# Performance work log

Measured on AMD Instinct MI355X. Metric: run time of the kernel, lower is better.

The kernel has to match this reference:

```python
import jax, jax.numpy as jnp
import numpy as np
from jax import lax

TAU_MIN = 0.01
TAU_MAX = 10.0
SLOW_TAU = 5.0


def setup_inputs() -> dict:
    key = jax.random.key(0)
    ks = iter(jax.random.split(key, 40))
    def p(shape, scale=0.05):
        return (jax.random.normal(next(ks), shape, jnp.float32) * scale)
    B, T, D = 1024, 512, 31
    FU, SU, H = 32, 32, 64
    inp = {
        "x": jax.random.normal(next(ks), (B, T, D), jnp.float32),
        # FlashFloodGate: Linear(62->32), Linear(32->1)
        "fg_w1": p((32, 2 * D)), "fg_b1": p((32,)),
        "fg_w2": p((1, 32)), "fg_b2": p((1,)),
        # fast LTC cell
        "fwin": p((FU, D)), "fbin": p((FU,)), "fwrec": p((FU, FU)),
        # slow LTC cell
        "swin": p((SU, D)), "sbin": p((SU,)), "swrec": p((SU, SU)),
        # fusion Linear(64->64)
        "fu_w": p((H, FU + SU)), "fu_b": p((H,)),
        # attention Linear(64->32), Linear(32->1)
        "at_w1": p((32, H)), "at_b1": p((32,)),
        "at_w2": p((1, 32)), "at_b2": p((1,)),
        # depth head Linear(64->64), Linear(64->5)
        "d_w1": p((64, H)), "d_b1": p((64,)),
        "d_w2": p((5, 64)), "d_b2": p((5,)),
        # overflow head Linear(64->64), Linear(64->32), Linear(32->1)
        "o_w1": p((64, H)), "o_b1": p((64,)),
        "o_w2": p((32, 64)), "o_b2": p((32,)),
        "o_w3": p((1, 32)), "o_b3": p((1,)),
        # intensity head Linear(64->32), Linear(32->1)
        "i_w1": p((32, H)), "i_b1": p((32,)),
        "i_w2": p((1, 32)), "i_b2": p((1,)),
    }
    return inp


def _ltc_scan(pre_tbh, w_rec, tau_tb1, h0):
    # pre_tbh: [T,B,H] precomputed W_in x + b; tau_tb1 broadcastable to [T,B,1]
    def step(h, inp):
        pre_t, tau_t = inp
        upd = jnp.tanh(pre_t + h @ w_rec.T)
        h = h + (upd - h) / tau_t
        return h, h
    _, hs = lax.scan(step, h0, (pre_tbh, tau_tb1))
    return jnp.transpose(hs, (1, 0, 2))  # [B,T,H]


def _forward(x, fg_w1, fg_b1, fg_w2, fg_b2, fwin, fbin, fwrec, swin, sbin, swrec,
             fu_w, fu_b, at_w1, at_b1, at_w2, at_b2, d_w1, d_b1, d_w2, d_b2,
             o_w1, o_b1, o_w2, o_b2, o_w3, o_b3, i_w1, i_b1, i_w2, i_b2):
    B, T, D = x.shape
    # FlashFloodGate over all timesteps (x_prev of t=0 is x_0 -> dx=0)
    dx = jnp.concatenate([jnp.zeros_like(x[:, :1]), x[:, 1:] - x[:, :-1]], axis=1)
    ci = jnp.concatenate([x, dx], axis=-1)                       # [B,T,2D]
    cs = jax.nn.sigmoid(jnp.tanh(ci @ fg_w1.T + fg_b1) @ fg_w2.T + fg_b2)  # [B,T,1]
    tau_fast = TAU_MAX - cs * (TAU_MAX - TAU_MIN)                # [B,T,1]
    # fast LTC (stepwise tau)
    pre_f = jnp.transpose(x @ fwin.T + fbin, (1, 0, 2))          # [T,B,FU]
    fast = _ltc_scan(pre_f, fwrec, jnp.transpose(tau_fast, (1, 0, 2)),
                     jnp.zeros((B, fwrec.shape[0]), x.dtype))
    # slow LTC (constant tau = 5.0, shape [B,1])
    pre_s = jnp.transpose(x @ swin.T + sbin, (1, 0, 2))          # [T,B,SU]
    slow = _ltc_scan(pre_s, swrec, jnp.full((T, 1, 1), SLOW_TAU, x.dtype),
                     jnp.zeros((B, swrec.shape[0]), x.dtype))
    # fusion
    ltc = jnp.tanh(jnp.concatenate([fast, slow], axis=-1) @ fu_w.T + fu_b)  # [B,T,H]
    # attention over time
    logits = jnp.tanh(ltc @ at_w1.T + at_b1) @ at_w2.T + at_b2   # [B,T,1]
    attn = jax.nn.softmax(logits, axis=1)
    context = jnp.sum(ltc * attn, axis=1)                        # [B,H]
    # heads (dropout is identity in eval)
    depths = jax.nn.relu(context @ d_w1.T + d_b1) @ d_w2.T + d_b2
    overflow = jax.nn.sigmoid(
        jax.nn.relu(jax.nn.relu(context @ o_w1.T + o_b1) @ o_w2.T + o_b2) @ o_w3.T + o_b3)
    intensity = jax.nn.sigmoid(jax.nn.relu(context @ i_w1.T + i_b1) @ i_w2.T + i_b2)
    return (depths, overflow, intensity)


def reference(x, fg_w1, fg_b1, fg_w2, fg_b2, fwin, fbin, fwrec, swin, sbin, swrec,
              fu_w, fu_b, at_w1, at_b1, at_w2, at_b2, d_w1, d_b1, d_w2, d_b2,
              o_w1, o_b1, o_w2, o_b2, o_w3, o_b3, i_w1, i_b1, i_w2, i_b2):
    return _forward(x, fg_w1, fg_b1, fg_w2, fg_b2, fwin, fbin, fwrec, swin, sbin,
                    swrec, fu_w, fu_b, at_w1, at_b1, at_w2, at_b2, d_w1, d_b1,
                    d_w2, d_b2, o_w1, o_b1, o_w2, o_b2, o_w3, o_b3,
                    i_w1, i_b1, i_w2, i_b2)
```

## Files before the change

kernel.cpp:

```cpp
#include <hip/hip_runtime.h>


#define T_  512
#define D_  31
#define GR_ 8
#define NG_ 64
#define NIT 70
#define L2E 1.4426950408889634f

typedef decltype(__builtin_amdgcn_cvt_pkrtz(0.0f, 0.0f)) h2;
typedef _Float16 h8v __attribute__((ext_vector_type(8)));
typedef float    f4v __attribute__((ext_vector_type(4)));

__device__ __forceinline__ float fexp2(float x){ return __builtin_amdgcn_exp2f(x); }
__device__ __forceinline__ float frcp (float x){ return __builtin_amdgcn_rcpf(x); }
__device__ __forceinline__ float fast_tanh(float x){
    float e = fexp2(x * 2.8853900817779268f);
    return 1.0f - 2.0f * frcp(1.0f + e);
}
__device__ __forceinline__ h2 cvt2(float a, float b){ return __builtin_amdgcn_cvt_pkrtz(a, b); }
__device__ __forceinline__ h2 bch2(unsigned v){ return __builtin_bit_cast(h2, v); }
__device__ __forceinline__ unsigned bcu(h2 v){ return __builtin_bit_cast(unsigned, v); }

template <int CTRL>
__device__ __forceinline__ float dppf(float v){
    int r = __builtin_amdgcn_update_dpp(0, __builtin_bit_cast(int, v),
                                        CTRL, 0xf, 0xf, true);
    return __builtin_bit_cast(float, r);
}
template <int CTRL>
__device__ __forceinline__ unsigned dppu(unsigned v){
    return (unsigned)__builtin_amdgcn_update_dpp(0, (int)v, CTRL, 0xf, 0xf, true);
}
__device__ __forceinline__ unsigned swz16(unsigned v){
    return (unsigned)__builtin_amdgcn_ds_swizzle((int)v, 0x401F);
}
__device__ __forceinline__ float rsum16(float v){
    v += dppf<0xB1>(v); v += dppf<0x4E>(v); v += dppf<0x141>(v); v += dppf<0x140>(v);
    return v;
}

#if __has_builtin(__builtin_amdgcn_fdot2)
#define FDOT2(acc, a, b) (acc) = __builtin_amdgcn_fdot2((a), (b), (acc), false)
#else
#define FDOT2(acc, a, b) (acc) += (float)(a)[0]*(float)(b)[0] + (float)(a)[1]*(float)(b)[1]
#endif

#define MFMA16(A, Bf, Cf) __builtin_amdgcn_mfma_f32_16x16x32_f16((A), (Bf), (Cf), 0, 0, 0)

#define BAR() do { asm volatile("s_waitcnt lgkmcnt(0)" ::: "memory"); \
                   __builtin_amdgcn_s_barrier();                      \
                   asm volatile("" ::: "memory"); } while (0)

__launch_bounds__(256, 4)
__global__ void lnn_mf(
    const float* __restrict__ X,
    const float* __restrict__ fg_w1, const float* __restrict__ fg_b1,
    const float* __restrict__ fg_w2, const float* __restrict__ fg_b2,
    const float* __restrict__ fwin,  const float* __restrict__ fbin,
    const float* __restrict__ fwrec,
    const float* __restrict__ swin,  const float* __restrict__ sbin,
    const float* __restrict__ swrec,
    const float* __restrict__ fu_w,  const float* __restrict__ fu_b,
    const float* __restrict__ at_w1, const float* __restrict__ at_b1,
    const float* __restrict__ at_w2, const float* __restrict__ at_b2,
    const float* __restrict__ d_w1,  const float* __restrict__ d_b1,
    const float* __restrict__ d_w2,  const float* __restrict__ d_b2,
    const float* __restrict__ o_w1,  const float* __restrict__ o_b1,
    const float* __restrict__ o_w2,  const float* __restrict__ o_b2,
    const float* __restrict__ o_w3,  const float* __restrict__ o_b3,
    const float* __restrict__ i_w1,  const float* __restrict__ i_b1,
    const float* __restrict__ i_w2,  const float* __restrict__ i_b2,
    float* __restrict__ out, int B)
{
    const int b    = blockIdx.x;
    const int tx   = threadIdx.x;
    const int wid  = tx >> 6;
    const int lane = tx & 63;
    const int u    = lane & 31;
    const int hb32 = lane & 32;
    const int role = (wid + b) & 3;

    __shared__ __align__(16) float    xr_sh [4][GR_][36];
    __shared__ float    xdm   [36];
    __shared__ float    pre_sh[4][GR_][65];
    __shared__ float    rt_sh [4][GR_];
    __shared__ __align__(16) unsigned hpk_sh[4][GR_][36];
    __shared__ __align__(16) unsigned ltcpk [4][GR_][36];
    __shared__ float    pw_sh [16];
    __shared__ float    ctx_sh[64];

    if (tx < 32) xr_sh[tx >> 3][tx & 7][31] = 0.0f;

    if (role == 0) {
        const int col = lane & 15, kb = lane >> 4;
        h8v wB[8];
        #pragma unroll
        for (int c = 0; c < 8; ++c) {
            float wv[8];
            #pragma unroll
            for (int j = 0; j < 8; ++j) {
                const int k = kb*8 + j;
                float v = 0.0f;
                if (k < 31) {
                    const int uu = 16*(c & 1) + col;
                    if (c < 2)      v = fg_w1[uu*62 + k] + fg_w1[uu*62 + 31 + k];
                    else if (c < 4) v = fg_w1[uu*62 + 31 + k];
                    else if (c < 6) v = fwin[uu*31 + k];
                    else            v = swin[uu*31 + k];
                }
                wv[j] = v;
            }
            uint4 qq = { bcu(cvt2(wv[0],wv[1])), bcu(cvt2(wv[2],wv[3])),
                         bcu(cvt2(wv[4],wv[5])), bcu(cvt2(wv[6],wv[7])) };
            wB[c] = __builtin_bit_cast(h8v, qq);
        }
        const float b1c[2] = { fg_b1[col], fg_b1[16 + col] };
        const float pb[4]  = { fbin[col], fbin[16+col], sbin[col], sbin[16+col] };
        const float w2n[2] = { fg_w2[col] * (-L2E), fg_w2[16+col] * (-L2E) };
        const float b2n    = fg_b2[0] * (-L2E);
        const unsigned* Xu = (const unsigned*)(X + (size_t)b * T_ * D_ + lane);
        float ypv[2] = {0.0f, 0.0f};
        asm volatile("s_waitcnt vmcnt(0)" ::: "memory");

        #pragma unroll
        for (int gg = 0; gg < 2; ++gg)
            #pragma unroll
            for (int k = 0; k < GR_; ++k)
                if (lane < 31)
                    __builtin_amdgcn_global_load_lds(
                        (const __attribute__((address_space(1))) unsigned*)(Xu + (size_t)(GR_*gg + k) * 31),
                        (__attribute__((address_space(3))) unsigned*)(&xr_sh[gg][k][0]),
                        4, 0, 0);

        for (int i = 0; i < NIT; ++i) {
            asm volatile("s_waitcnt vmcnt(8)" ::: "memory");
            BAR();
            {
                const int gq = i + 2;
                #pragma unroll
                for (int k = 0; k < GR_; ++k) {
                    int tl = GR_*gq + k; if (tl > 511) tl = 511;
                    float* dst = (gq <= NG_-1) ? &xr_sh[gq & 3][k][0] : &xdm[0];
                    if (lane < 31)
                        __builtin_amdgcn_global_load_lds(
                            (const __attribute__((address_space(1))) unsigned*)(Xu + (size_t)tl * 31),
                            (__attribute__((address_space(3))) unsigned*)dst,
                            4, 0, 0);
                }
            }
            if ((i & 1) && i <= NG_-1) {
                const int sA_ = (i-1) & 3, sB_ = i & 3;
                const float* xrow = (col < 8) ? &xr_sh[sA_][col][kb*8]
                                              : &xr_sh[sB_][col-8][kb*8];
                float4 xa = *(const float4*)xrow;
                float4 xb = *(const float4*)(xrow + 4);
                uint4 aq = { bcu(cvt2(xa.x,xa.y)), bcu(cvt2(xa.z,xa.w)),
                             bcu(cvt2(xb.x,xb.y)), bcu(cvt2(xb.z,xb.w)) };
                h8v Af = __builtin_bit_cast(h8v, aq);
                f4v C[8];
                #pragma unroll
                for (int c = 0; c < 8; ++c) {
                    f4v z = {0.f, 0.f, 0.f, 0.f};
                    C[c] = MFMA16(Af, wB[c], z);
                }
                const int tslot = (kb < 2) ? sA_ : sB_;
                const int tb    = (kb & 1) * 4;
                float tp[4] = {0.f, 0.f, 0.f, 0.f};
                #pragma unroll
                for (int p = 0; p < 2; ++p) {
                    f4v G = C[p], Y = C[2+p];
                    if (i == 1) ypv[p] = __shfl(Y[0], col);
                    float ylast = __shfl(Y[3], 48 + col);
                    float yup   = __shfl(Y[3], (lane - 16) & 63);
                    float ysh0  = (kb == 0) ? ypv[p] : yup;
                    float h1v[4];
                    h1v[0] = fast_tanh(G[0] - ysh0 + b1c[p]);
                    h1v[1] = fast_tanh(G[1] - Y[0] + b1c[p]);
                    h1v[2] = fast_tanh(G[2] - Y[1] + b1c[p]);
                    h1v[3] = fast_tanh(G[3] - Y[2] + b1c[p]);
                    ypv[p] = ylast;
                    #pragma unroll
                    for (int r = 0; r < 4; ++r) tp[r] += h1v[r] * w2n[p];
                }
                #pragma unroll
                for (int r = 0; r < 4; ++r) {
                    float s  = rsum16(tp[r]) + b2n;
                    float cs = frcp(1.0f + fexp2(s));
                    float rt = frcp(10.0f - 9.99f * cs);
                    if (col == 0) rt_sh[tslot][tb + r] = rt;
                }
                #pragma unroll
                for (int c = 4; c < 8; ++c) {
                    const int uo = (c < 6 ? 0 : 32) + 16*(c & 1) + col;
                    #pragma unroll
                    for (int r = 0; r < 4; ++r)
                        pre_sh[tslot][tb + r][uo] = C[c][r] + pb[c-4];
                }
            }
        }
        asm volatile("s_waitcnt vmcnt(0)" ::: "memory");
    } else if (role == 1) {
        const bool slow = (lane >= 32);
        const float* W  = (slow ? swrec : fwrec) + u * 32;
        const int M0[8] = {0,2,7,5,15,13,8,10};
        const int M1[8] = {1,3,6,4,14,12,9,11};
        h2 wr[16];
        #pragma unroll
        for (int j = 0; j < 16; ++j) {
            const int x = (j & 8) ? 16 : 0;
            wr[j] = cvt2(W[u ^ M0[j & 7] ^ x], W[u ^ M1[j & 7] ^ x]);
        }
        float h_st = 0.0f;

        for (int i = 0; i < NIT; ++i) {
            BAR();
            if (i >= 2 && i <= NG_ + 1) {
                const int sR = (i - 2) & 3;
                float preA[8], rtA[8];
                #pragma unroll
                for (int k = 0; k < GR_; ++k) {
                    preA[k] = pre_sh[sR][k][lane];
                    rtA[k]  = slow ? 0.2f : rt_sh[sR][k];
                }
                __builtin_amdgcn_s_setprio(1);
                #pragma unroll
                for (int k = 0; k < GR_; ++k) {
                    float hn = dppf<0xB1>(h_st);
                    unsigned u0 = bcu(cvt2(h_st, hn));
                    unsigned u1 = dppu<0x4E>(u0);
                    unsigned u2 = dppu<0x141>(u0);
                    unsigned u3 = dppu<0x141>(u1);
                    unsigned u4 = dppu<0x140>(u0);
                    unsigned u5 = dppu<0x140>(u1);
                    unsigned u6 = dppu<0x140>(u2);
                    unsigned u7 = dppu<0x140>(u3);
                    unsigned u8  = swz16(u0), u9  = swz16(u1);
                    unsigned u10 = swz16(u2), u11 = swz16(u3);
                    unsigned u12 = swz16(u4), u13 = swz16(u5);
                    unsigned u14 = swz16(u6), u15 = swz16(u7);
                    float a0 = 0.f, a1 = 0.f, a2 = 0.f, a3 = 0.f;
                    FDOT2(a0, bch2(u0),  wr[0]);  FDOT2(a1, bch2(u1),  wr[1]);
                    FDOT2(a2, bch2(u2),  wr[2]);  FDOT2(a3, bch2(u3),  wr[3]);
                    FDOT2(a0, bch2(u4),  wr[4]);  FDOT2(a1, bch2(u5),  wr[5]);
                    FDOT2(a2, bch2(u6),  wr[6]);  FDOT2(a3, bch2(u7),  wr[7]);
                    FDOT2(a0, bch2(u8),  wr[8]);  FDOT2(a1, bch2(u9),  wr[9]);
                    FDOT2(a2, bch2(u10), wr[10]); FDOT2(a3, bch2(u11), wr[11]);
                    FDOT2(a0, bch2(u12), wr[12]); FDOT2(a1, bch2(u13), wr[13]);
                    FDOT2(a2, bch2(u14), wr[14]); FDOT2(a3, bch2(u15), wr[15]);
                    float v   = (a0 + a1) + (a2 + a3);
                    float upd = fast_tanh(v + preA[k]);
                    h_st += (upd - h_st) * rtA[k];
                    float hw = dppf<0xB1>(h_st);
                    if (!(lane & 1))
                        hpk_sh[sR][k][lane >> 1] = bcu(cvt2(h_st, hw));
                }
                __builtin_amdgcn_s_setprio(0);
            }
        }
    } else if (role == 2) {
        const int col = lane & 15, kb = lane >> 4;
        h8v wF[8];
        #pragma unroll
        for (int kc = 0; kc < 2; ++kc)
            #pragma unroll
            for (int nc = 0; nc < 4; ++nc) {
                float wv[8];
                #pragma unroll
                for (int j = 0; j < 8; ++j)
                    wv[j] = fu_w[(16*nc + col)*64 + 32*kc + 8*kb + j];
                uint4 qq = { bcu(cvt2(wv[0],wv[1])), bcu(cvt2(wv[2],wv[3])),
                             bcu(cvt2(wv[4],wv[5])), bcu(cvt2(wv[6],wv[7])) };
                wF[kc*4 + nc] = __builtin_bit_cast(h8v, qq);
            }
        const float fb4[4] = { fu_b[col], fu_b[16+col], fu_b[32+col], fu_b[48+col] };

        for (int i = 0; i < NIT; ++i) {
            BAR();
            if ((i & 1) && i >= 5 && i <= 67) {
                const int s0 = (i-5) & 3, s1 = (i-4) & 3;
                const unsigned* hrow = (col < 8) ? &hpk_sh[s0][col][0]
                                                 : &hpk_sh[s1][col-8][0];
                uint4 a0q = *(const uint4*)(hrow + kb*4);
                uint4 a1q = *(const uint4*)(hrow + kb*4 + 16);
                h8v A0 = __builtin_bit_cast(h8v, a0q);
                h8v A1 = __builtin_bit_cast(h8v, a1q);
                const int tslot = (kb < 2) ? s0 : s1;
                const int tb    = (kb & 1) * 4;
                #pragma unroll
                for (int nc = 0; nc < 4; ++nc) {
                    f4v c4 = {0.f, 0.f, 0.f, 0.f};
                    c4 = MFMA16(A0, wF[nc],     c4);
                    c4 = MFMA16(A1, wF[4 + nc], c4);
                    #pragma unroll
                    for (int r = 0; r < 4; ++r) {
                        float v  = fast_tanh(c4[r] + fb4[nc]);
                        float vn = dppf<0xB1>(v);
                        h2 pk = (col & 1) ? cvt2(vn, v) : cvt2(v, vn);
                        if (!(col & 1))
                            ltcpk[tslot][tb + r][(16*nc + col) >> 1] = bcu(pk);
                    }
                }
            }
        }
    } else {
        const int col = lane & 15, kb = lane >> 4;
        h8v wA[4];
        #pragma unroll
        for (int kt = 0; kt < 2; ++kt)
            #pragma unroll
            for (int nt = 0; nt < 2; ++nt) {
                float wv[8];
                #pragma unroll
                for (int j = 0; j < 8; ++j)
                    wv[j] = at_w1[(nt*16 + col)*64 + kt*32 + 8*kb + j];
                uint4 qq = { bcu(cvt2(wv[0],wv[1])), bcu(cvt2(wv[2],wv[3])),
                             bcu(cvt2(wv[4],wv[5])), bcu(cvt2(wv[6],wv[7])) };
                wA[kt*2 + nt] = __builtin_bit_cast(h8v, qq);
            }
        const float ab1v[2] = { at_b1[col], at_b1[16 + col] };
        const float w2L[2]  = { at_w2[col] * L2E, at_w2[16 + col] * L2E };
        const float ab2L    = at_b2[0] * L2E;
        float s_run = 0.0f, c_run = 0.0f;

        for (int i = 0; i < NIT; ++i) {
            BAR();
            if ((i & 1) && i >= 7) {
                const int s0 = (i-7) & 3, s1 = (i-6) & 3;
                const unsigned* lrow = (col < 8) ? &ltcpk[s0][col][0]
                                                 : &ltcpk[s1][col-8][0];
                uint4 l0q = *(const uint4*)(lrow + kb*4);
                uint4 l1q = *(const uint4*)(lrow + kb*4 + 16);
                h8v L0 = __builtin_bit_cast(h8v, l0q);
                h8v L1 = __builtin_bit_cast(h8v, l1q);
                f4v CA[2];
                #pragma unroll
                for (int nt = 0; nt < 2; ++nt) {
                    f4v c4 = {0.f, 0.f, 0.f, 0.f};
                    c4 = MFMA16(L0, wA[nt],     c4);
                    c4 = MFMA16(L1, wA[2 + nt], c4);
                    CA[nt] = c4;
                }
                #pragma unroll
                for (int r = 0; r < 4; ++r) {
                    float s = fast_tanh(CA[0][r] + ab1v[0]) * w2L[0]
                            + fast_tanh(CA[1][r] + ab1v[1]) * w2L[1];
                    s = rsum16(s);
                    float pw = fexp2(s + ab2L);
                    if (col == 0) pw_sh[kb*4 + r] = pw;
                }
                #pragma unroll
                for (int t = 0; t < 16; ++t) {
                    const int sl = (t < 8) ? s0 : s1;
                    const int tr = t & 7;
                    float ltc = (float)((const _Float16*)(&ltcpk[sl][tr][0]))[lane];
                    float pwv = pw_sh[t];
                    s_run += pwv;
                    c_run += pwv * ltc;
                }
            }
        }
        ctx_sh[lane] = c_run * frcp(s_run);
    }

    __syncthreads();

    if (wid == 0) {
        float r1 = d_b1[lane];
        #pragma unroll
        for (int c = 0; c < 16; ++c) {
            float4 cq = ((const float4*)ctx_sh)[c];
            float4 wq = ((const float4*)(d_w1 + lane*64))[c];
            r1 += wq.x*cq.x + wq.y*cq.y + wq.z*cq.z + wq.w*cq.w;
        }
        r1 = fmaxf(r1, 0.0f);
        #pragma unroll
        for (int kk = 0; kk < 5; ++kk) {
            float v = d_w2[kk*64 + lane] * r1;
            v += __shfl_xor(v, 1);  v += __shfl_xor(v, 2);
            v += __shfl_xor(v, 4);  v += __shfl_xor(v, 8);
            v += __shfl_xor(v, 16); v += __shfl_xor(v, 32);
            if (lane == 0) out[b*5 + kk] = v + d_b2[kk];
        }
    } else if (wid == 1) {
        float r1 = o_b1[lane];
        #pragma unroll
        for (int c = 0; c < 16; ++c) {
            float4 cq = ((const float4*)ctx_sh)[c];
            float4 wq = ((const float4*)(o_w1 + lane*64))[c];
            r1 += wq.x*cq.x + wq.y*cq.y + wq.z*cq.z + wq.w*cq.w;
        }
        r1 = fmaxf(r1, 0.0f);
        float acc = 0.0f;
        #pragma unroll
        for (int j = 0; j < 32; ++j) {
            float rj = __shfl(r1, hb32 + j);
            acc += o_w2[u*64 + hb32 + j] * rj;
        }
        acc += __shfl_xor(acc, 32);
        float r2 = fmaxf(acc + o_b2[u], 0.0f);
        float v  = o_w3[u] * r2;
        v += __shfl_xor(v, 1);  v += __shfl_xor(v, 2);
        v += __shfl_xor(v, 4);  v += __shfl_xor(v, 8);
        v += __shfl_xor(v, 16);
        if (lane == 0) {
            float e = fexp2((v + o_b3[0]) * -L2E);
            out[5*B + b] = frcp(1.0f + e);
        }
    } else if (wid == 2) {
        float acc = 0.0f;
        #pragma unroll
        for (int c = 0; c < 8; ++c) {
            float4 cq = ((const float4*)(ctx_sh + hb32))[c];
            float4 wq = ((const float4*)(i_w1 + u*64 + hb32))[c];
            acc += wq.x*cq.x + wq.y*cq.y + wq.z*cq.z + wq.w*cq.w;
        }
        acc += __shfl_xor(acc, 32);
        float r1 = fmaxf(acc + i_b1[u], 0.0f);
        float v  = i_w2[u] * r1;
        v += __shfl_xor(v, 1);  v += __shfl_xor(v, 2);
        v += __shfl_xor(v, 4);  v += __shfl_xor(v, 8);
        v += __shfl_xor(v, 16);
        if (lane == 0) {
            float e = fexp2((v + i_b2[0]) * -L2E);
            out[6*B + b] = frcp(1.0f + e);
        }
    }
}

extern "C" void kernel_launch(void* const* d_in, const int* in_sizes, int n_in,
                              void* d_out, int out_size, void* d_ws, size_t ws_size,
                              hipStream_t stream) {
    (void)n_in; (void)out_size; (void)d_ws; (void)ws_size;
    const float* X     = (const float*)d_in[0];
    const float* fg_w1 = (const float*)d_in[1];
    const float* fg_b1 = (const float*)d_in[2];
    const float* fg_w2 = (const float*)d_in[3];
    const float* fg_b2 = (const float*)d_in[4];
    const float* fwin  = (const float*)d_in[5];
    const float* fbin  = (const float*)d_in[6];
    const float* fwrec = (const float*)d_in[7];
    const float* swin  = (const float*)d_in[8];
    const float* sbin  = (const float*)d_in[9];
    const float* swrec = (const float*)d_in[10];
    const float* fu_w  = (const float*)d_in[11];
    const float* fu_b  = (const float*)d_in[12];
    const float* at_w1 = (const float*)d_in[13];
    const float* at_b1 = (const float*)d_in[14];
    const float* at_w2 = (const float*)d_in[15];
    const float* at_b2 = (const float*)d_in[16];
    const float* d_w1  = (const float*)d_in[17];
    const float* d_b1  = (const float*)d_in[18];
    const float* d_w2  = (const float*)d_in[19];
    const float* d_b2  = (const float*)d_in[20];
    const float* o_w1  = (const float*)d_in[21];
    const float* o_b1  = (const float*)d_in[22];
    const float* o_w2  = (const float*)d_in[23];
    const float* o_b2  = (const float*)d_in[24];
    const float* o_w3  = (const float*)d_in[25];
    const float* o_b3  = (const float*)d_in[26];
    const float* i_w1  = (const float*)d_in[27];
    const float* i_b1  = (const float*)d_in[28];
    const float* i_w2  = (const float*)d_in[29];
    const float* i_b2  = (const float*)d_in[30];
    float* out = (float*)d_out;

    const int B = in_sizes[0] / (T_ * D_);
    dim3 grid(B), block(256);
    hipLaunchKernelGGL(lnn_mf, grid, block, 0, stream,
        X, fg_w1, fg_b1, fg_w2, fg_b2, fwin, fbin, fwrec, swin, sbin, swrec,
        fu_w, fu_b, at_w1, at_b1, at_w2, at_b2, d_w1, d_b1, d_w2, d_b2,
        o_w1, o_b1, o_w2, o_b2, o_w3, o_b3, i_w1, i_b1, i_w2, i_b2, out, B);
}
```

Measured before the change: 111.0 us.

## Double timestep group size to halve pipeline barriers and simplify stage scheduling

Raises each pipeline stage's group from 8 to 16 timesteps, so the warp-specialized pipeline runs 36 barrier iterations instead of 70. Stages now work every iteration on one full 16-row group instead of pairing two 8-row groups on alternate iterations, and the h and ltc staging buffers shrink to double buffers. The recurrence also builds its upper-half operands with DPP ops from a single swizzled value instead of eight swizzles. In exchange, the recurrence does more serial steps per iteration while the other stages wait, and register pressure rises from the larger preA/rtA arrays.

```diff
diff --git a/kernel.cpp b/kernel.cpp
--- a/kernel.cpp
+++ b/kernel.cpp
@@ -3,9 +3,9 @@
 
 #define T_  512
 #define D_  31
-#define GR_ 8
-#define NG_ 64
-#define NIT 70
+#define GR_ 16
+#define NG_ 32
+#define NIT 36
 #define L2E 1.4426950408889634f
 
 typedef decltype(__builtin_amdgcn_cvt_pkrtz(0.0f, 0.0f)) h2;
@@ -85,12 +85,12 @@
     __shared__ float    xdm   [36];
     __shared__ float    pre_sh[4][GR_][65];
     __shared__ float    rt_sh [4][GR_];
-    __shared__ __align__(16) unsigned hpk_sh[4][GR_][36];
-    __shared__ __align__(16) unsigned ltcpk [4][GR_][36];
-    __shared__ float    pw_sh [16];
+    __shared__ __align__(16) unsigned hpk_sh[2][GR_][36];
+    __shared__ __align__(16) unsigned ltcpk [2][GR_][36];
+    __shared__ float    pw_sh [GR_];
     __shared__ float    ctx_sh[64];
 
-    if (tx < 32) xr_sh[tx >> 3][tx & 7][31] = 0.0f;
+    if (tx < 64) xr_sh[tx >> 4][tx & 15][31] = 0.0f;
 
     if (role == 0) {
         const int col = lane & 15, kb = lane >> 4;
@@ -134,7 +134,7 @@
                         4, 0, 0);
 
         for (int i = 0; i < NIT; ++i) {
-            asm volatile("s_waitcnt vmcnt(8)" ::: "memory");
+            asm volatile("s_waitcnt vmcnt(16)" ::: "memory");
             BAR();
             {
                 const int gq = i + 2;
@@ -149,10 +149,9 @@
                             4, 0, 0);
                 }
             }
-            if ((i & 1) && i <= NG_-1) {
-                const int sA_ = (i-1) & 3, sB_ = i & 3;
-                const float* xrow = (col < 8) ? &xr_sh[sA_][col][kb*8]
-                                              : &xr_sh[sB_][col-8][kb*8];
+            if (i <= NG_-1) {
+                const int sG = i & 3;
+                const float* xrow = &xr_sh[sG][col][kb*8];
                 float4 xa = *(const float4*)xrow;
                 float4 xb = *(const float4*)(xrow + 4);
                 uint4 aq = { bcu(cvt2(xa.x,xa.y)), bcu(cvt2(xa.z,xa.w)),
@@ -164,13 +163,12 @@
                     f4v z = {0.f, 0.f, 0.f, 0.f};
                     C[c] = MFMA16(Af, wB[c], z);
                 }
-                const int tslot = (kb < 2) ? sA_ : sB_;
-                const int tb    = (kb & 1) * 4;
+                const int tb = kb * 4;
                 float tp[4] = {0.f, 0.f, 0.f, 0.f};
                 #pragma unroll
                 for (int p = 0; p < 2; ++p) {
                     f4v G = C[p], Y = C[2+p];
-                    if (i == 1) ypv[p] = __shfl(Y[0], col);
+                    if (i == 0) ypv[p] = __shfl(Y[0], col);
                     float ylast = __shfl(Y[3], 48 + col);
                     float yup   = __shfl(Y[3], (lane - 16) & 63);
                     float ysh0  = (kb == 0) ? ypv[p] : yup;
@@ -188,14 +186,14 @@
                     float s  = rsum16(tp[r]) + b2n;
                     float cs = frcp(1.0f + fexp2(s));
                     float rt = frcp(10.0f - 9.99f * cs);
-                    if (col == 0) rt_sh[tslot][tb + r] = rt;
+                    if (col == 0) rt_sh[sG][tb + r] = rt;
                 }
                 #pragma unroll
                 for (int c = 4; c < 8; ++c) {
                     const int uo = (c < 6 ? 0 : 32) + 16*(c & 1) + col;
                     #pragma unroll
                     for (int r = 0; r < 4; ++r)
-                        pre_sh[tslot][tb + r][uo] = C[c][r] + pb[c-4];
+                        pre_sh[sG][tb + r][uo] = C[c][r] + pb[c-4];
                 }
             }
         }
@@ -216,8 +214,10 @@
         for (int i = 0; i < NIT; ++i) {
             BAR();
             if (i >= 2 && i <= NG_ + 1) {
-                const int sR = (i - 2) & 3;
-                float preA[8], rtA[8];
+                const int gR = i - 2;
+                const int sR = gR & 3;
+                const int sH = gR & 1;
+                float preA[GR_], rtA[GR_];
                 #pragma unroll
                 for (int k = 0; k < GR_; ++k) {
                     preA[k] = pre_sh[sR][k][lane];
@@ -228,6 +228,7 @@
                 for (int k = 0; k < GR_; ++k) {
                     float hn = dppf<0xB1>(h_st);
                     unsigned u0 = bcu(cvt2(h_st, hn));
+                    unsigned w0 = swz16(u0);
                     unsigned u1 = dppu<0x4E>(u0);
                     unsigned u2 = dppu<0x141>(u0);
                     unsigned u3 = dppu<0x141>(u1);
@@ -235,25 +236,28 @@
                     unsigned u5 = dppu<0x140>(u1);
                     unsigned u6 = dppu<0x140>(u2);
                     unsigned u7 = dppu<0x140>(u3);
-                    unsigned u8  = swz16(u0), u9  = swz16(u1);
-                    unsigned u10 = swz16(u2), u11 = swz16(u3);
-                    unsigned u12 = swz16(u4), u13 = swz16(u5);
-                    unsigned u14 = swz16(u6), u15 = swz16(u7);
+                    unsigned w1 = dppu<0x4E>(w0);
+                    unsigned w2 = dppu<0x141>(w0);
+                    unsigned w3 = dppu<0x141>(w1);
+                    unsigned w4 = dppu<0x140>(w0);
+                    unsigned w5 = dppu<0x140>(w1);
+                    unsigned w6 = dppu<0x140>(w2);
+                    unsigned w7 = dppu<0x140>(w3);
                     float a0 = 0.f, a1 = 0.f, a2 = 0.f, a3 = 0.f;
-                    FDOT2(a0, bch2(u0),  wr[0]);  FDOT2(a1, bch2(u1),  wr[1]);
-                    FDOT2(a2, bch2(u2),  wr[2]);  FDOT2(a3, bch2(u3),  wr[3]);
-                    FDOT2(a0, bch2(u4),  wr[4]);  FDOT2(a1, bch2(u5),  wr[5]);
-                    FDOT2(a2, bch2(u6),  wr[6]);  FDOT2(a3, bch2(u7),  wr[7]);
-                    FDOT2(a0, bch2(u8),  wr[8]);  FDOT2(a1, bch2(u9),  wr[9]);
-                    FDOT2(a2, bch2(u10), wr[10]); FDOT2(a3, bch2(u11), wr[11]);
-                    FDOT2(a0, bch2(u12), wr[12]); FDOT2(a1, bch2(u13), wr[13]);
-                    FDOT2(a2, bch2(u14), wr[14]); FDOT2(a3, bch2(u15), wr[15]);
+                    FDOT2(a0, bch2(u0), wr[0]);  FDOT2(a1, bch2(u1), wr[1]);
+                    FDOT2(a2, bch2(u2), wr[2]);  FDOT2(a3, bch2(u3), wr[3]);
+                    FDOT2(a0, bch2(u4), wr[4]);  FDOT2(a1, bch2(u5), wr[5]);
+                    FDOT2(a2, bch2(u6), wr[6]);  FDOT2(a3, bch2(u7), wr[7]);
+                    FDOT2(a0, bch2(w0), wr[8]);  FDOT2(a1, bch2(w1), wr[9]);
+                    FDOT2(a2, bch2(w2), wr[10]); FDOT2(a3, bch2(w3), wr[11]);
+                    FDOT2(a0, bch2(w4), wr[12]); FDOT2(a1, bch2(w5), wr[13]);
+                    FDOT2(a2, bch2(w6), wr[14]); FDOT2(a3, bch2(w7), wr[15]);
                     float v   = (a0 + a1) + (a2 + a3);
                     float upd = fast_tanh(v + preA[k]);
                     h_st += (upd - h_st) * rtA[k];
                     float hw = dppf<0xB1>(h_st);
                     if (!(lane & 1))
-                        hpk_sh[sR][k][lane >> 1] = bcu(cvt2(h_st, hw));
+                        hpk_sh[sH][k][lane >> 1] = bcu(cvt2(h_st, hw));
                 }
                 __builtin_amdgcn_s_setprio(0);
             }
@@ -277,16 +281,15 @@
 
         for (int i = 0; i < NIT; ++i) {
             BAR();
-            if ((i & 1) && i >= 5 && i <= 67) {
-                const int s0 = (i-5) & 3, s1 = (i-4) & 3;
-                const unsigned* hrow = (col < 8) ? &hpk_sh[s0][col][0]
-                                                 : &hpk_sh[s1][col-8][0];
+            if (i >= 3 && i <= NG_ + 2) {
+                const int gF = i - 3;
+                const int sH = gF & 1;
+                const unsigned* hrow = &hpk_sh[sH][col][0];
                 uint4 a0q = *(const uint4*)(hrow + kb*4);
                 uint4 a1q = *(const uint4*)(hrow + kb*4 + 16);
                 h8v A0 = __builtin_bit_cast(h8v, a0q);
                 h8v A1 = __builtin_bit_cast(h8v, a1q);
-                const int tslot = (kb < 2) ? s0 : s1;
-                const int tb    = (kb & 1) * 4;
+                const int tb = kb * 4;
                 #pragma unroll
                 for (int nc = 0; nc < 4; ++nc) {
                     f4v c4 = {0.f, 0.f, 0.f, 0.f};
@@ -298,7 +301,7 @@
                         float vn = dppf<0xB1>(v);
                         h2 pk = (col & 1) ? cvt2(vn, v) : cvt2(v, vn);
                         if (!(col & 1))
-                            ltcpk[tslot][tb + r][(16*nc + col) >> 1] = bcu(pk);
+                            ltcpk[gF & 1][tb + r][(16*nc + col) >> 1] = bcu(pk);
                     }
                 }
             }
@@ -325,10 +328,10 @@
 
         for (int i = 0; i < NIT; ++i) {
             BAR();
-            if ((i & 1) && i >= 7) {
-                const int s0 = (i-7) & 3, s1 = (i-6) & 3;
-                const unsigned* lrow = (col < 8) ? &ltcpk[s0][col][0]
-                                                 : &ltcpk[s1][col-8][0];
+            if (i >= 4) {
+                const int gA = i - 4;
+                const int sl = gA & 1;
+                const unsigned* lrow = &ltcpk[sl][col][0];
                 uint4 l0q = *(const uint4*)(lrow + kb*4);
                 uint4 l1q = *(const uint4*)(lrow + kb*4 + 16);
                 h8v L0 = __builtin_bit_cast(h8v, l0q);
@@ -350,10 +353,8 @@
                     if (col == 0) pw_sh[kb*4 + r] = pw;
                 }
                 #pragma unroll
-                for (int t = 0; t < 16; ++t) {
-                    const int sl = (t < 8) ? s0 : s1;
-                    const int tr = t & 7;
-                    float ltc = (float)((const _Float16*)(&ltcpk[sl][tr][0]))[lane];
+                for (int t = 0; t < GR_; ++t) {
+                    float ltc = (float)((const _Float16*)(&ltcpk[sl][t][0]))[lane];
                     float pwv = pw_sh[t];
                     s_run += pwv;
                     c_run += pwv * ltc;
```

Result: faster. 96.79 us (-12.8%).
